# Kernel optimization log

Measured on AMD Instinct MI355X. Metric: run time of the kernel, lower is better.

The kernel has to match this reference:

```python
import jax, jax.numpy as jnp
import numpy as np

B, T, D, E, WR, H = 4, 2048, 1024, 4, 128, 4096  # batch, seq, d_model, mem_experts, read width, fuse hidden
EPS = 1e-5


def _ln(u, g, b):
    mu = jnp.mean(u, axis=-1, keepdims=True)
    var = jnp.mean(jnp.square(u - mu), axis=-1, keepdims=True)
    return (u - mu) * jax.lax.rsqrt(var + EPS) * g + b


def setup_inputs() -> dict:
    key = jax.random.key(0)
    ks = jax.random.split(key, 8)
    s1 = 1.0 / np.sqrt(D + WR)
    s2 = 1.0 / np.sqrt(H)
    sg = 1.0 / np.sqrt((1 + E) * D)
    return {
        "x": jax.random.normal(ks[0], (B, T, D), jnp.float32),
        "vt": jax.random.normal(ks[1], (B, T, D), jnp.float32),
        "dts": jax.random.normal(ks[2], (E, B, T, D), jnp.float32),
        "r_feat": jax.random.normal(ks[3], (B, T, WR), jnp.float32),
        "fuse_ln_g": jnp.ones((D + WR,), jnp.float32),
        "fuse_ln_b": jnp.zeros((D + WR,), jnp.float32),
        "fuse_w1": jax.random.normal(ks[4], (D + WR, H), jnp.float32) * s1,
        "fuse_b1": jnp.zeros((H,), jnp.float32),
        "fuse_w2": jax.random.normal(ks[5], (H, D), jnp.float32) * s2,
        "fuse_b2": jnp.zeros((D,), jnp.float32),
        "pg_ln_g": jnp.ones(((1 + E) * D,), jnp.float32),
        "pg_ln_b": jnp.zeros(((1 + E) * D,), jnp.float32),
        "gate_w": jax.random.normal(ks[6], ((1 + E) * D, 1 + E), jnp.float32) * sg,
        "gate_b": jnp.concatenate([jnp.zeros((1,)), jnp.full((E,), -1.0)]).astype(jnp.float32),
    }


def reference(x, vt, dts, r_feat, fuse_ln_g, fuse_ln_b, fuse_w1, fuse_b1,
              fuse_w2, fuse_b2, pg_ln_g, pg_ln_b, gate_w, gate_b):
    # fusion branch: vt = vt + MLP(LN(cat(x, read_feat)))
    fuse_in = jnp.concatenate([x, r_feat], axis=-1)            # [B,T,D+WR]
    h = jax.nn.gelu(_ln(fuse_in, fuse_ln_g, fuse_ln_b) @ fuse_w1 + fuse_b1)
    vt = vt + (h @ fuse_w2 + fuse_b2)

    # paths = [vanilla] + mem experts -> [P,B,T,D], P = 1+E
    paths = jnp.concatenate([vt[None], dts], axis=0)
    z = jnp.moveaxis(paths, 0, -2).reshape(x.shape[0], x.shape[1], -1)  # cat over last dim
    logits = _ln(z, pg_ln_g, pg_ln_b) @ gate_w + gate_b        # temp = 1.0
    pi = jax.nn.softmax(logits, axis=-1)                        # [B,T,P]

    out = jnp.einsum('btp,pbtd->btd', pi, paths)
    g_mem = jnp.sum(pi[..., 1:], axis=-1, keepdims=True)        # synthetic memory gate
    return out, g_mem
```

## Files before the change

kernel.cpp:

```cpp
#include <hip/hip_runtime.h>
#include <hip/hip_bf16.h>

#define Bc 4
#define Tc 2048
#define Dc 1024
#define Ec 4
#define WRc 128
#define Hc 4096
#define Mc (Bc*Tc)
#define K1c (Dc+WRc)
#define Pc (1+Ec)
#define ZDc (Pc*Dc)
#define EPSc 1e-5f

typedef __attribute__((ext_vector_type(8))) short short8;
typedef __attribute__((ext_vector_type(4))) short short4v;
typedef __attribute__((ext_vector_type(4))) float f32x4;

__device__ __forceinline__ float wave_red_sum(float v) {
    #pragma unroll
    for (int o = 32; o > 0; o >>= 1) v += __shfl_down(v, o);
    return v;
}

__device__ __forceinline__ float gelu_tanh(float x) {
    const float c = 0.7978845608028654f;
    float x3 = x * x * x;
    return 0.5f * x * (1.0f + tanhf(c * (x + 0.044715f * x3)));
}

__device__ __forceinline__ void store_bf16x4(__hip_bfloat16* p, f32x4 v) {
    __hip_bfloat16 t[4];
    t[0] = __float2bfloat16(v[0]); t[1] = __float2bfloat16(v[1]);
    t[2] = __float2bfloat16(v[2]); t[3] = __float2bfloat16(v[3]);
    *(short4v*)p = *(const short4v*)t;
}

__global__ __launch_bounds__(256) void transpose_cast_kernel(
    const float* __restrict__ src, __hip_bfloat16* __restrict__ dst, int R, int C) {
    __shared__ float tile[32][33];
    int c0 = blockIdx.x * 32, r0 = blockIdx.y * 32;
    int tx = threadIdx.x, ty = threadIdx.y;
    #pragma unroll
    for (int i = ty; i < 32; i += 8)
        tile[i][tx] = src[(size_t)(r0 + i) * C + c0 + tx];
    __syncthreads();
    #pragma unroll
    for (int i = ty; i < 32; i += 8)
        dst[(size_t)(c0 + i) * R + r0 + tx] = __float2bfloat16(tile[tx][i]);
}

__global__ __launch_bounds__(256) void gwT_kernel(
    const float* __restrict__ gw, float* __restrict__ gwT) {
    int i = blockIdx.x * 256 + threadIdx.x;
    #pragma unroll
    for (int j = 0; j < Pc; j++) gwT[j * ZDc + i] = gw[i * Pc + j];
}

__global__ __launch_bounds__(256) void fuse_ln_kernel(
    const float* __restrict__ x, const float* __restrict__ rf,
    const float* __restrict__ g, const float* __restrict__ b,
    __hip_bfloat16* __restrict__ aln) {
    int row = blockIdx.x;
    int tid = threadIdx.x, lane = tid & 63, wave = tid >> 6;
    const f32x4* x4 = (const f32x4*)(x + (size_t)row * Dc);
    const f32x4* r4 = (const f32x4*)(rf + (size_t)row * WRc);

    f32x4 v0 = x4[tid];
    f32x4 v1 = {0.f, 0.f, 0.f, 0.f};
    if (tid < 32) v1 = r4[tid];

    float s  = v0[0]+v0[1]+v0[2]+v0[3] + v1[0]+v1[1]+v1[2]+v1[3];
    float s2 = v0[0]*v0[0]+v0[1]*v0[1]+v0[2]*v0[2]+v0[3]*v0[3]
             + v1[0]*v1[0]+v1[1]*v1[1]+v1[2]*v1[2]+v1[3]*v1[3];

    __shared__ float red[8];
    float sw = wave_red_sum(s), s2w = wave_red_sum(s2);
    if (lane == 0) { red[wave] = sw; red[4 + wave] = s2w; }
    __syncthreads();
    float stot  = red[0] + red[1] + red[2] + red[3];
    float s2tot = red[4] + red[5] + red[6] + red[7];
    const float inv = 1.0f / (float)K1c;
    float mu = stot * inv;
    float var = s2tot * inv - mu * mu;
    float rstd = rsqrtf(var + EPSc);

    __hip_bfloat16* orow = aln + (size_t)row * K1c;
    {
        f32x4 gg = *(const f32x4*)(g + tid * 4);
        f32x4 bb = *(const f32x4*)(b + tid * 4);
        f32x4 o  = (v0 - mu) * rstd * gg + bb;
        store_bf16x4(orow + tid * 4, o);
    }
    if (tid < 32) {
        f32x4 gg = *(const f32x4*)(g + 1024 + tid * 4);
        f32x4 bb = *(const f32x4*)(b + 1024 + tid * 4);
        f32x4 o  = (v1 - mu) * rstd * gg + bb;
        store_bf16x4(orow + 1024 + tid * 4, o);
    }
}

template <int Mdim, int Ndim, int Kdim, int BN, int EPI>
__global__ __launch_bounds__(256) void gemm_kernel(
    const __hip_bfloat16* __restrict__ A, const __hip_bfloat16* __restrict__ Bt,
    const float* __restrict__ bias, const float* __restrict__ add,
    void* __restrict__ outp) {
    constexpr int BM = 128, BK = 64;
    constexpr int WN = BN / 2;
    constexpr int MF = 4, NF = WN / 16;
    constexpr int NTN = Ndim / BN;
    constexpr int NT  = (Mdim / BM) * NTN;
    constexpr int GB  = BN * 8 / 256;

    __shared__ __hip_bfloat16 As[BM * BK];
    __shared__ __hip_bfloat16 Bs[BN * BK];

    const int tid  = threadIdx.x;
    const int lane = tid & 63;
    const int wave = tid >> 6;
    const int wr = wave >> 1, wc = wave & 1;

    constexpr int CPX = NT / 8;
    int bid = blockIdx.x;
    int swz = (bid & 7) * CPX + (bid >> 3);
    const int m0 = (swz / NTN) * BM;
    const int n0 = (swz % NTN) * BN;

    const __hip_bfloat16* ag = A  + (size_t)(m0 + (tid >> 3)) * Kdim + (tid & 7) * 8;
    const __hip_bfloat16* bg = Bt + (size_t)(n0 + (tid >> 3)) * Kdim + (tid & 7) * 8;

    f32x4 acc[MF][NF] = {};

    for (int k0 = 0; k0 < Kdim; k0 += BK) {
        __syncthreads();
        #pragma unroll
        for (int i = 0; i < 4; i++)
            __builtin_amdgcn_global_load_lds(
                (const __attribute__((address_space(1))) void*)(ag + (size_t)i * 32 * Kdim),
                (__attribute__((address_space(3))) void*)(As + (i * 256 + tid) * 8), 16, 0, 0);
        #pragma unroll
        for (int i = 0; i < GB; i++)
            __builtin_amdgcn_global_load_lds(
                (const __attribute__((address_space(1))) void*)(bg + (size_t)i * 32 * Kdim),
                (__attribute__((address_space(3))) void*)(Bs + (i * 256 + tid) * 8), 16, 0, 0);
        ag += BK; bg += BK;
        __syncthreads();

        #pragma unroll
        for (int kk = 0; kk < 2; kk++) {
            short8 af[MF], bf[NF];
            #pragma unroll
            for (int m = 0; m < MF; m++)
                af[m] = *(const short8*)(As + (wr * 64 + m * 16 + (lane & 15)) * BK + kk * 32 + (lane >> 4) * 8);
            #pragma unroll
            for (int n = 0; n < NF; n++)
                bf[n] = *(const short8*)(Bs + (wc * WN + n * 16 + (lane & 15)) * BK + kk * 32 + (lane >> 4) * 8);
            #pragma unroll
            for (int m = 0; m < MF; m++)
                #pragma unroll
                for (int n = 0; n < NF; n++)
                    acc[m][n] = __builtin_amdgcn_mfma_f32_16x16x32_bf16(af[m], bf[n], acc[m][n], 0, 0, 0);
        }
    }

    #pragma unroll
    for (int m = 0; m < MF; m++) {
        int grow_base = m0 + wr * 64 + m * 16 + (lane >> 4) * 4;
        #pragma unroll
        for (int n = 0; n < NF; n++) {
            int gcol = n0 + wc * WN + n * 16 + (lane & 15);
            float bv = bias[gcol];
            #pragma unroll
            for (int i = 0; i < 4; i++) {
                int grow = grow_base + i;
                float vv = acc[m][n][i] + bv;
                if (EPI == 0) {
                    ((__hip_bfloat16*)outp)[(size_t)grow * Ndim + gcol] = __float2bfloat16(gelu_tanh(vv));
                } else {
                    ((float*)outp)[(size_t)grow * Ndim + gcol] = vv + add[(size_t)grow * Ndim + gcol];
                }
            }
        }
    }
}

__global__ __launch_bounds__(256) void gate_kernel(
    const float* __restrict__ vtn, const float* __restrict__ dts,
    const float* __restrict__ g, const float* __restrict__ b,
    const float* __restrict__ gwT, const float* __restrict__ gb,
    float* __restrict__ out, float* __restrict__ gmem) {
    int row = blockIdx.x;
    int tid = threadIdx.x, lane = tid & 63, wave = tid >> 6;
    __shared__ f32x4 z4[ZDc / 4];
    __shared__ float red[8];
    __shared__ float lsum[Pc];
    if (tid < Pc) lsum[tid] = 0.f;

    const f32x4* vt4 = (const f32x4*)(vtn + (size_t)row * Dc);
    float s = 0.f, s2 = 0.f;
    #pragma unroll
    for (int k = 0; k < 5; k++) {
        int i4 = tid + k * 256;
        int p  = i4 >> 8;
        int d4 = i4 & 255;
        f32x4 u = (p == 0) ? vt4[d4]
                : *(const f32x4*)(dts + ((size_t)(p - 1) * Mc + row) * Dc + d4 * 4);
        z4[i4] = u;
        s  += u[0] + u[1] + u[2] + u[3];
        s2 += u[0]*u[0] + u[1]*u[1] + u[2]*u[2] + u[3]*u[3];
    }
    float sw = wave_red_sum(s), s2w = wave_red_sum(s2);
    if (lane == 0) { red[wave] = sw; red[4 + wave] = s2w; }
    __syncthreads();
    float stot  = red[0] + red[1] + red[2] + red[3];
    float s2tot = red[4] + red[5] + red[6] + red[7];
    const float inv = 1.0f / (float)ZDc;
    float mu = stot * inv;
    float var = s2tot * inv - mu * mu;
    float rstd = rsqrtf(var + EPSc);

    float lacc[Pc] = {0.f, 0.f, 0.f, 0.f, 0.f};
    #pragma unroll
    for (int k = 0; k < 5; k++) {
        int i4 = tid + k * 256;
        f32x4 zz = z4[i4];
        f32x4 gg = *(const f32x4*)(g + i4 * 4);
        f32x4 bb = *(const f32x4*)(b + i4 * 4);
        f32x4 zh = (zz - mu) * rstd * gg + bb;
        #pragma unroll
        for (int j = 0; j < Pc; j++) {
            f32x4 w = *(const f32x4*)(gwT + j * ZDc + i4 * 4);
            lacc[j] += zh[0]*w[0] + zh[1]*w[1] + zh[2]*w[2] + zh[3]*w[3];
        }
    }
    #pragma unroll
    for (int j = 0; j < Pc; j++) {
        float v = wave_red_sum(lacc[j]);
        if (lane == 0) atomicAdd(&lsum[j], v);
    }
    __syncthreads();

    float lg[Pc];
    #pragma unroll
    for (int j = 0; j < Pc; j++) lg[j] = lsum[j] + gb[j];
    float mx = lg[0];
    #pragma unroll
    for (int j = 1; j < Pc; j++) mx = fmaxf(mx, lg[j]);
    float ex[Pc], den = 0.f;
    #pragma unroll
    for (int j = 0; j < Pc; j++) { ex[j] = expf(lg[j] - mx); den += ex[j]; }
    float rden = 1.0f / den;
    float pi[Pc];
    #pragma unroll
    for (int j = 0; j < Pc; j++) pi[j] = ex[j] * rden;

    f32x4 o = {0.f, 0.f, 0.f, 0.f};
    #pragma unroll
    for (int p = 0; p < Pc; p++) o += pi[p] * z4[p * 256 + tid];
    *(f32x4*)(out + (size_t)row * Dc + tid * 4) = o;
    if (tid == 0) gmem[row] = pi[1] + pi[2] + pi[3] + pi[4];
}

extern "C" void kernel_launch(void* const* d_in, const int* in_sizes, int n_in,
                              void* d_out, int out_size, void* d_ws, size_t ws_size,
                              hipStream_t stream) {
    const float* x    = (const float*)d_in[0];
    const float* vt   = (const float*)d_in[1];
    const float* dts  = (const float*)d_in[2];
    const float* rf   = (const float*)d_in[3];
    const float* flg  = (const float*)d_in[4];
    const float* flb  = (const float*)d_in[5];
    const float* w1   = (const float*)d_in[6];
    const float* b1   = (const float*)d_in[7];
    const float* w2   = (const float*)d_in[8];
    const float* b2   = (const float*)d_in[9];
    const float* plg  = (const float*)d_in[10];
    const float* plb  = (const float*)d_in[11];
    const float* gw   = (const float*)d_in[12];
    const float* gb   = (const float*)d_in[13];

    char* ws = (char*)d_ws;
    size_t off = 0;
    __hip_bfloat16* w1t = (__hip_bfloat16*)(ws + off); off += (size_t)Hc * K1c * 2;
    __hip_bfloat16* w2t = (__hip_bfloat16*)(ws + off); off += (size_t)Dc * Hc * 2;
    __hip_bfloat16* aln = (__hip_bfloat16*)(ws + off); off += (size_t)Mc * K1c * 2;
    __hip_bfloat16* h   = (__hip_bfloat16*)(ws + off); off += (size_t)Mc * Hc * 2;
    float*          vtn = (float*)(ws + off);          off += (size_t)Mc * Dc * 4;
    float*          gwT = (float*)(ws + off);          off += (size_t)Pc * ZDc * 4;

    transpose_cast_kernel<<<dim3(Hc / 32, K1c / 32), dim3(32, 8), 0, stream>>>(w1, w1t, K1c, Hc);
    transpose_cast_kernel<<<dim3(Dc / 32, Hc / 32), dim3(32, 8), 0, stream>>>(w2, w2t, Hc, Dc);
    gwT_kernel<<<ZDc / 256, 256, 0, stream>>>(gw, gwT);

    fuse_ln_kernel<<<Mc, 256, 0, stream>>>(x, rf, flg, flb, aln);

    gemm_kernel<Mc, Hc, K1c, 128, 0><<<(Mc / 128) * (Hc / 128), 256, 0, stream>>>(
        aln, w1t, b1, nullptr, h);

    gemm_kernel<Mc, Dc, Hc, 64, 1><<<(Mc / 128) * (Dc / 64), 256, 0, stream>>>(
        h, w2t, b2, vt, vtn);

    float* outp = (float*)d_out;
    gate_kernel<<<Mc, 256, 0, stream>>>(vtn, dts, plg, plb, gwT, gb, outp, outp + (size_t)Mc * Dc);
}
```

Before: 602.0 us.

## Triple-buffer GEMM with async LDS loads, XOR swizzle, larger tiles; register-cache gate rows

Replaces the single-buffered GEMM with a 256x128 tile, 512-thread kernel that triple-buffers A/B tiles in LDS. It prefetches two K-steps ahead with direct global-to-LDS loads, using explicit vmcnt waits and barriers. An XOR swizzle on the LDS column index is meant to avoid bank conflicts on fragment reads. The gate kernel keeps each thread's five path vectors in registers instead of staging them through shared memory. Risks include higher LDS and register use lowering occupancy, and correctness depending on the hand-tuned vmcnt counts.

```diff
diff --git a/kernel.cpp b/kernel.cpp
--- a/kernel.cpp
+++ b/kernel.cpp
@@ -100,20 +100,20 @@
     }
 }
 
-template <int Mdim, int Ndim, int Kdim, int BN, int EPI>
-__global__ __launch_bounds__(256) void gemm_kernel(
+template <int Mdim, int Ndim, int Kdim, int EPI>
+__global__ __launch_bounds__(512, 2) void gemm_pipe_kernel(
     const __hip_bfloat16* __restrict__ A, const __hip_bfloat16* __restrict__ Bt,
     const float* __restrict__ bias, const float* __restrict__ add,
     void* __restrict__ outp) {
-    constexpr int BM = 128, BK = 64;
-    constexpr int WN = BN / 2;
-    constexpr int MF = 4, NF = WN / 16;
+    constexpr int BM = 256, BN = 128, BK = 64;
+    constexpr int NTK = Kdim / BK;
     constexpr int NTN = Ndim / BN;
     constexpr int NT  = (Mdim / BM) * NTN;
-    constexpr int GB  = BN * 8 / 256;
-
-    __shared__ __hip_bfloat16 As[BM * BK];
-    __shared__ __hip_bfloat16 Bs[BN * BK];
+    constexpr int ATILE = BM * BK;
+    constexpr int BTILE = BN * BK;
+
+    __shared__ __hip_bfloat16 As[3 * ATILE];
+    __shared__ __hip_bfloat16 Bs[3 * BTILE];
 
     const int tid  = threadIdx.x;
     const int lane = tid & 63;
@@ -126,49 +126,87 @@
     const int m0 = (swz / NTN) * BM;
     const int n0 = (swz % NTN) * BN;
 
-    const __hip_bfloat16* ag = A  + (size_t)(m0 + (tid >> 3)) * Kdim + (tid & 7) * 8;
-    const __hip_bfloat16* bg = Bt + (size_t)(n0 + (tid >> 3)) * Kdim + (tid & 7) * 8;
-
-    f32x4 acc[MF][NF] = {};
-
-    for (int k0 = 0; k0 < Kdim; k0 += BK) {
-        __syncthreads();
+    const int srow  = tid >> 3;
+    const int scolg = (tid & 7) ^ (srow & 7);
+    const __hip_bfloat16* aSrc = A  + (size_t)(m0 + srow) * Kdim + scolg * 8;
+    const __hip_bfloat16* bSrc = Bt + (size_t)(n0 + srow) * Kdim + scolg * 8;
+
+    auto stage = [&](int t) {
+        const __hip_bfloat16* ap = aSrc + (size_t)t * BK;
+        const __hip_bfloat16* bp = bSrc + (size_t)t * BK;
+        __hip_bfloat16* ad = As + (t % 3) * ATILE + tid * 8;
+        __hip_bfloat16* bd = Bs + (t % 3) * BTILE + tid * 8;
         #pragma unroll
         for (int i = 0; i < 4; i++)
             __builtin_amdgcn_global_load_lds(
-                (const __attribute__((address_space(1))) void*)(ag + (size_t)i * 32 * Kdim),
-                (__attribute__((address_space(3))) void*)(As + (i * 256 + tid) * 8), 16, 0, 0);
-        #pragma unroll
-        for (int i = 0; i < GB; i++)
+                (const __attribute__((address_space(1))) void*)(ap + (size_t)i * 64 * Kdim),
+                (__attribute__((address_space(3))) void*)(ad + i * 4096), 16, 0, 0);
+        #pragma unroll
+        for (int i = 0; i < 2; i++)
             __builtin_amdgcn_global_load_lds(
-                (const __attribute__((address_space(1))) void*)(bg + (size_t)i * 32 * Kdim),
-                (__attribute__((address_space(3))) void*)(Bs + (i * 256 + tid) * 8), 16, 0, 0);
-        ag += BK; bg += BK;
-        __syncthreads();
-
+                (const __attribute__((address_space(1))) void*)(bp + (size_t)i * 64 * Kdim),
+                (__attribute__((address_space(3))) void*)(bd + i * 4096), 16, 0, 0);
+    };
+
+    f32x4 acc[4][4] = {};
+
+    auto compute = [&](int t) {
+        const __hip_bfloat16* Ab = As + (t % 3) * ATILE;
+        const __hip_bfloat16* Bb = Bs + (t % 3) * BTILE;
         #pragma unroll
         for (int kk = 0; kk < 2; kk++) {
-            short8 af[MF], bf[NF];
+            short8 af[4], bf[4];
             #pragma unroll
-            for (int m = 0; m < MF; m++)
-                af[m] = *(const short8*)(As + (wr * 64 + m * 16 + (lane & 15)) * BK + kk * 32 + (lane >> 4) * 8);
+            for (int m = 0; m < 4; m++) {
+                int row = wr * 64 + m * 16 + (lane & 15);
+                int col = (kk * 32 + (lane >> 4) * 8) ^ ((row & 7) << 3);
+                af[m] = *(const short8*)(Ab + row * 64 + col);
+            }
             #pragma unroll
-            for (int n = 0; n < NF; n++)
-                bf[n] = *(const short8*)(Bs + (wc * WN + n * 16 + (lane & 15)) * BK + kk * 32 + (lane >> 4) * 8);
+            for (int n = 0; n < 4; n++) {
+                int row = wc * 64 + n * 16 + (lane & 15);
+                int col = (kk * 32 + (lane >> 4) * 8) ^ ((row & 7) << 3);
+                bf[n] = *(const short8*)(Bb + row * 64 + col);
+            }
             #pragma unroll
-            for (int m = 0; m < MF; m++)
+            for (int m = 0; m < 4; m++)
                 #pragma unroll
-                for (int n = 0; n < NF; n++)
+                for (int n = 0; n < 4; n++)
                     acc[m][n] = __builtin_amdgcn_mfma_f32_16x16x32_bf16(af[m], bf[n], acc[m][n], 0, 0, 0);
         }
-    }
-
-    #pragma unroll
-    for (int m = 0; m < MF; m++) {
+    };
+
+    stage(0);
+    stage(1);
+    for (int t = 0; t < NTK - 2; ++t) {
+        stage(t + 2);
+        asm volatile("s_waitcnt vmcnt(12)" ::: "memory");
+        __builtin_amdgcn_sched_barrier(0);
+        __builtin_amdgcn_s_barrier();
+        __builtin_amdgcn_sched_barrier(0);
+        compute(t);
+        __builtin_amdgcn_sched_barrier(0);
+        __builtin_amdgcn_s_barrier();
+        __builtin_amdgcn_sched_barrier(0);
+    }
+    asm volatile("s_waitcnt vmcnt(6)" ::: "memory");
+    __builtin_amdgcn_sched_barrier(0);
+    __builtin_amdgcn_s_barrier();
+    __builtin_amdgcn_sched_barrier(0);
+    compute(NTK - 2);
+    __builtin_amdgcn_sched_barrier(0);
+    __builtin_amdgcn_s_barrier();
+    __builtin_amdgcn_sched_barrier(0);
+    asm volatile("s_waitcnt vmcnt(0)" ::: "memory");
+    __builtin_amdgcn_sched_barrier(0);
+    compute(NTK - 1);
+
+    #pragma unroll
+    for (int m = 0; m < 4; m++) {
         int grow_base = m0 + wr * 64 + m * 16 + (lane >> 4) * 4;
         #pragma unroll
-        for (int n = 0; n < NF; n++) {
-            int gcol = n0 + wc * WN + n * 16 + (lane & 15);
+        for (int n = 0; n < 4; n++) {
+            int gcol = n0 + wc * 64 + n * 16 + (lane & 15);
             float bv = bias[gcol];
             #pragma unroll
             for (int i = 0; i < 4; i++) {
@@ -191,23 +229,21 @@
     float* __restrict__ out, float* __restrict__ gmem) {
     int row = blockIdx.x;
     int tid = threadIdx.x, lane = tid & 63, wave = tid >> 6;
-    __shared__ f32x4 z4[ZDc / 4];
     __shared__ float red[8];
     __shared__ float lsum[Pc];
     if (tid < Pc) lsum[tid] = 0.f;
 
-    const f32x4* vt4 = (const f32x4*)(vtn + (size_t)row * Dc);
+    f32x4 v[Pc];
+    v[0] = *(const f32x4*)(vtn + (size_t)row * Dc + tid * 4);
+    #pragma unroll
+    for (int p = 1; p < Pc; p++)
+        v[p] = *(const f32x4*)(dts + ((size_t)(p - 1) * Mc + row) * Dc + tid * 4);
+
     float s = 0.f, s2 = 0.f;
     #pragma unroll
-    for (int k = 0; k < 5; k++) {
-        int i4 = tid + k * 256;
-        int p  = i4 >> 8;
-        int d4 = i4 & 255;
-        f32x4 u = (p == 0) ? vt4[d4]
-                : *(const f32x4*)(dts + ((size_t)(p - 1) * Mc + row) * Dc + d4 * 4);
-        z4[i4] = u;
-        s  += u[0] + u[1] + u[2] + u[3];
-        s2 += u[0]*u[0] + u[1]*u[1] + u[2]*u[2] + u[3]*u[3];
+    for (int p = 0; p < Pc; p++) {
+        s  += v[p][0] + v[p][1] + v[p][2] + v[p][3];
+        s2 += v[p][0]*v[p][0] + v[p][1]*v[p][1] + v[p][2]*v[p][2] + v[p][3]*v[p][3];
     }
     float sw = wave_red_sum(s), s2w = wave_red_sum(s2);
     if (lane == 0) { red[wave] = sw; red[4 + wave] = s2w; }
@@ -221,12 +257,11 @@
 
     float lacc[Pc] = {0.f, 0.f, 0.f, 0.f, 0.f};
     #pragma unroll
-    for (int k = 0; k < 5; k++) {
-        int i4 = tid + k * 256;
-        f32x4 zz = z4[i4];
+    for (int p = 0; p < Pc; p++) {
+        int i4 = p * 256 + tid;
         f32x4 gg = *(const f32x4*)(g + i4 * 4);
         f32x4 bb = *(const f32x4*)(b + i4 * 4);
-        f32x4 zh = (zz - mu) * rstd * gg + bb;
+        f32x4 zh = (v[p] - mu) * rstd * gg + bb;
         #pragma unroll
         for (int j = 0; j < Pc; j++) {
             f32x4 w = *(const f32x4*)(gwT + j * ZDc + i4 * 4);
@@ -235,8 +270,8 @@
     }
     #pragma unroll
     for (int j = 0; j < Pc; j++) {
-        float v = wave_red_sum(lacc[j]);
-        if (lane == 0) atomicAdd(&lsum[j], v);
+        float vv = wave_red_sum(lacc[j]);
+        if (lane == 0) atomicAdd(&lsum[j], vv);
     }
     __syncthreads();
 
@@ -256,7 +291,7 @@
 
     f32x4 o = {0.f, 0.f, 0.f, 0.f};
     #pragma unroll
-    for (int p = 0; p < Pc; p++) o += pi[p] * z4[p * 256 + tid];
+    for (int p = 0; p < Pc; p++) o += pi[p] * v[p];
     *(f32x4*)(out + (size_t)row * Dc + tid * 4) = o;
     if (tid == 0) gmem[row] = pi[1] + pi[2] + pi[3] + pi[4];
 }
@@ -294,10 +329,10 @@
 
     fuse_ln_kernel<<<Mc, 256, 0, stream>>>(x, rf, flg, flb, aln);
 
-    gemm_kernel<Mc, Hc, K1c, 128, 0><<<(Mc / 128) * (Hc / 128), 256, 0, stream>>>(
+    gemm_pipe_kernel<Mc, Hc, K1c, 0><<<(Mc / 256) * (Hc / 128), 512, 0, stream>>>(
         aln, w1t, b1, nullptr, h);
 
-    gemm_kernel<Mc, Dc, Hc, 64, 1><<<(Mc / 128) * (Dc / 64), 256, 0, stream>>>(
+    gemm_pipe_kernel<Mc, Dc, Hc, 1><<<(Mc / 256) * (Dc / 128), 512, 0, stream>>>(
         h, w2t, b2, vt, vtn);
 
     float* outp = (float*)d_out;
```

Measured after the change: 550.5 us. 1.09x faster.
